# Kernel tuning notes

Hardware: AMD Instinct MI355X
Metric: run time of the kernel (lower is better)

Reference implementation:

```python
import jax, jax.numpy as jnp
import numpy as np

TOP_K = 2
NUM_EXPERTS = 64
TEMPERATURE = 3.0           # buffer initial value (moe_routing_temperature default)
LOAD_BALANCE_ALPHA = 0.01
Z_LOSS_ALPHA = 1e-4


def setup_inputs() -> dict:
    key = jax.random.key(0)
    k1, k2 = jax.random.split(key)
    B, S, H, E = 4, 4096, 4096, NUM_EXPERTS
    x = jax.random.normal(k1, (B, S, H), dtype=jnp.float32)
    gate_w = jax.random.normal(k2, (E, H), dtype=jnp.float32) * (1.0 / np.sqrt(H))
    expert_bias = jnp.zeros((E,), dtype=jnp.float32)
    return {"x": x, "gate_w": gate_w, "expert_bias": expert_bias}


def reference(x, gate_w, expert_bias):
    # Eval-mode path: no noise, no warmup scaling, static top_k, seq_len < 8192
    # -> logits scaled by the temperature buffer.
    B, S, H = x.shape
    E = gate_w.shape[0]
    x_flat = x.reshape(-1, H)                               # [T, H], T = B*S
    logits = jnp.einsum('th,eh->te', x_flat, gate_w) + expert_bias  # [T, E]
    logits = logits / TEMPERATURE
    probs = jax.nn.softmax(logits, axis=-1)                 # [T, E]
    top_scores, top_idx = jax.lax.top_k(probs, TOP_K)       # [T, K]
    top_scores = top_scores / jnp.sum(top_scores, axis=-1, keepdims=True)
    # Load-balance aux loss: fraction of routed tokens per expert * mean prob.
    sel_counts = jax.nn.one_hot(top_idx, E, dtype=logits.dtype).sum(axis=1)  # [T, E]
    frac_routed = sel_counts.mean(axis=0)                   # [E], sums to TOP_K
    mean_prob = probs.mean(axis=0)                          # [E]
    lb_loss = LOAD_BALANCE_ALPHA * E * jnp.sum(frac_routed * mean_prob)
    # Z-loss for routing stability.
    z_loss = Z_LOSS_ALPHA * jnp.mean(jax.nn.logsumexp(logits, axis=-1) ** 2)
    total_loss = lb_loss + z_loss
    return top_scores, top_idx, total_loss
```

## Files before the change

### kernel.cpp

```cpp
#include <hip/hip_runtime.h>
#include <hip/hip_bf16.h>
#include <math.h>

typedef float f32x4 __attribute__((ext_vector_type(4)));
typedef short bf16x8 __attribute__((ext_vector_type(8)));

#define H_DIM 4096
#define E_EXP 64
#define NTOK  16384
#define PLANE (E_EXP * H_DIM)
#define PS    132
#define NBLK  256

__device__ __forceinline__ void split8(f32x4 a, f32x4 b, bf16x8 &h, bf16x8 &m, bf16x8 &l){
#pragma unroll
    for (int j = 0; j < 8; j++){
        float v = (j < 4) ? a[j] : b[j - 4];
        __hip_bfloat16 hb = __float2bfloat16(v);
        float r1 = v - __bfloat162float(hb);
        __hip_bfloat16 mb = __float2bfloat16(r1);
        float r2 = r1 - __bfloat162float(mb);
        __hip_bfloat16 lb = __float2bfloat16(r2);
        h[j] = __builtin_bit_cast(short, hb);
        m[j] = __builtin_bit_cast(short, mb);
        l[j] = __builtin_bit_cast(short, lb);
    }
}

#define MFMA __builtin_amdgcn_mfma_f32_16x16x32_bf16

__device__ __forceinline__ void gload_lds(const short* g, char* l){
    __builtin_amdgcn_global_load_lds(
        (const __attribute__((address_space(1))) void*)g,
        (__attribute__((address_space(3))) void*)l, 16, 0, 0);
}

__global__ __launch_bounds__(256) void moe_wsplit(
    const float* __restrict__ gw, short* __restrict__ wpl)
{
    const int idx = (blockIdx.x * 256 + threadIdx.x) * 8;
    f32x4 a = *(const f32x4*)(gw + idx);
    f32x4 b = *(const f32x4*)(gw + idx + 4);
    bf16x8 h, m, l; split8(a, b, h, m, l);
    *(bf16x8*)(wpl + idx)             = h;
    *(bf16x8*)(wpl + PLANE + idx)     = m;
    *(bf16x8*)(wpl + 2 * PLANE + idx) = l;
}

__global__ __launch_bounds__(256, 3) void moe_gate_main(
    const float* __restrict__ x, const short* __restrict__ wpl,
    const float* __restrict__ bias, float* __restrict__ out,
    float* __restrict__ part)
{
    __shared__ short wlds[12288];
    __shared__ float ls[64 * 68];
    __shared__ float bs[64], rs[64], zW[4];
    __shared__ int   ia[64], ib[64];

    const int tid = threadIdx.x, bid = blockIdx.x;
    const int wv = tid >> 6, l = tid & 63, l16 = l & 15, lk = l >> 4;
    const int tok0 = bid * 64;

    if (tid < 64) bs[tid] = bias[tid];

    const short* wsrc[3]; int wdst[3];
#pragma unroll
    for (int i = 0; i < 3; i++){
        const int sg = wv * 3 + i, p = sg >> 2, kg = sg & 3;
        wsrc[i] = wpl + p * PLANE + l * H_DIM + kg * 8;
        wdst[i] = p * 4096 + kg * 1024;
    }
    const int fb = lk * 1024 + l16 * 16;
    const float* xbase = x + (size_t)(tok0 + wv * 16 + l16) * H_DIM + lk * 8;

    f32x4 acc[4] = {};

#define STAGE(ccn, BUFW) do {                                               \
    __builtin_amdgcn_sched_barrier(0);                                      \
    _Pragma("unroll")                                                       \
    for (int i_ = 0; i_ < 3; i_++)                                          \
        gload_lds(wsrc[i_] + (ccn) * 32,                                    \
                  (char*)wlds + wdst[i_] + (BUFW) * 12288);                 \
    __builtin_amdgcn_sched_barrier(0);                                      \
} while(0)

#define KPHASE(cc, BUFR, XA, XB, XNA, XNB, DO_NEXT) do {                    \
    if (DO_NEXT) {                                                          \
        STAGE((cc) + 1, ((cc) + 1) & 1);                                    \
        XNA = *(const f32x4*)(xbase + ((cc) + 1) * 32);                     \
        XNB = *(const f32x4*)(xbase + ((cc) + 1) * 32 + 4);                 \
    }                                                                       \
    bf16x8 xh, xm, xl; split8(XA, XB, xh, xm, xl);                          \
    bf16x8 wf[4][3];                                                        \
    _Pragma("unroll")                                                       \
    for (int g_ = 0; g_ < 4; g_++)                                          \
        _Pragma("unroll")                                                   \
        for (int p_ = 0; p_ < 3; p_++)                                      \
            wf[g_][p_] = *(const bf16x8*)((char*)wlds + fb +                \
                           (BUFR) * 12288 + p_ * 4096 + g_ * 256);          \
    _Pragma("unroll")                                                       \
    for (int g_ = 0; g_ < 4; g_++){                                         \
        acc[g_] = MFMA(xh, wf[g_][0], acc[g_], 0, 0, 0);                    \
        acc[g_] = MFMA(xm, wf[g_][0], acc[g_], 0, 0, 0);                    \
        acc[g_] = MFMA(xh, wf[g_][1], acc[g_], 0, 0, 0);                    \
        acc[g_] = MFMA(xm, wf[g_][1], acc[g_], 0, 0, 0);                    \
        acc[g_] = MFMA(xh, wf[g_][2], acc[g_], 0, 0, 0);                    \
        acc[g_] = MFMA(xl, wf[g_][0], acc[g_], 0, 0, 0);                    \
    }                                                                       \
    if (DO_NEXT) {                                                          \
        asm volatile("s_waitcnt vmcnt(2)" ::: "memory");                    \
        __builtin_amdgcn_sched_barrier(0);                                  \
        __builtin_amdgcn_s_barrier();                                       \
    }                                                                       \
} while(0)

    STAGE(0, 0);
    f32x4 xeA = *(const f32x4*)(xbase);
    f32x4 xeB = *(const f32x4*)(xbase + 4);
    f32x4 xoA, xoB;
    asm volatile("s_waitcnt vmcnt(2)" ::: "memory");
    __builtin_amdgcn_sched_barrier(0);
    __builtin_amdgcn_s_barrier();

    for (int t = 0; t < 64; t++){
        KPHASE(2 * t,     0, xeA, xeB, xoA, xoB, true);
        KPHASE(2 * t + 1, 1, xoA, xoB, xeA, xeB, (t < 63));
    }

#pragma unroll
    for (int g = 0; g < 4; g++)
#pragma unroll
        for (int r = 0; r < 4; r++)
            ls[(16 * wv + lk * 4 + r) * 68 + g * 16 + l16] = acc[g][r];

    {
        const int t = tid >> 2, s4 = tid & 3, eb0 = s4 * 16;
        const float invTemp = (1.0f / 3.0f);
        float m1 = -1e30f, m2 = -1e30f; int i1 = 0, i2 = 0;
        for (int j = 0; j < 16; ++j){
            const int e = eb0 + j;
            float v = (ls[t * 68 + e] + bs[e]) * invTemp;
            ls[t * 68 + e] = v;
            if (v > m1)      { m2 = m1; i2 = i1; m1 = v; i1 = e; }
            else if (v > m2) { m2 = v;  i2 = e; }
        }
#pragma unroll
        for (int off = 1; off <= 2; off <<= 1){
            float om1 = __shfl_xor(m1, off), om2 = __shfl_xor(m2, off);
            int   oi1 = __shfl_xor(i1, off), oi2 = __shfl_xor(i2, off);
            bool sw = (om1 > m1) || (om1 == m1 && oi1 < i1);
            float n1 = sw ? om1 : m1;  int ni1 = sw ? oi1 : i1;
            float lm = sw ? m1  : om1; int li  = sw ? i1  : oi1;
            float w2 = sw ? om2 : m2;  int wi  = sw ? oi2 : i2;
            bool s2 = (lm > w2) || (lm == w2 && li < wi);
            m1 = n1; i1 = ni1;
            m2 = s2 ? lm : w2; i2 = s2 ? li : wi;
        }
        float ssum = 0.f;
        for (int j = 0; j < 16; ++j){
            const int e = eb0 + j;
            float p = __expf(ls[t * 68 + e] - m1);
            ls[t * 68 + e] = p;
            ssum += p;
        }
        ssum += __shfl_xor(ssum, 1);
        ssum += __shfl_xor(ssum, 2);

        float zsq = 0.f;
        if (s4 == 0){
            rs[t] = 1.0f / ssum; ia[t] = i1; ib[t] = i2;
            float p2    = __expf(m2 - m1);
            float inv12 = 1.0f / (1.0f + p2);
            out[(size_t)(tok0 + t) * 2 + 0] = inv12;
            out[(size_t)(tok0 + t) * 2 + 1] = p2 * inv12;
            out[(size_t)NTOK * 2 + (size_t)(tok0 + t) * 2 + 0] = (float)i1;
            out[(size_t)NTOK * 2 + (size_t)(tok0 + t) * 2 + 1] = (float)i2;
            float lse = m1 + logf(ssum);
            zsq = lse * lse;
        }
#pragma unroll
        for (int o = 32; o; o >>= 1) zsq += __shfl_xor(zsq, o);
        if ((tid & 63) == 0) zW[tid >> 6] = zsq;
    }
    __syncthreads();

    if (tid < 64){
        float psum = 0.f, csum = 0.f;
        for (int t2 = 0; t2 < 64; ++t2){
            psum += ls[t2 * 68 + tid] * rs[t2];
            csum += (ia[t2] == tid ? 1.f : 0.f) + (ib[t2] == tid ? 1.f : 0.f);
        }
        part[bid * PS + tid]      = psum;
        part[bid * PS + 64 + tid] = csum;
        if (tid == 0) part[bid * PS + 128] = zW[0] + zW[1] + zW[2] + zW[3];
    }
}

__global__ __launch_bounds__(1024) void moe_gate_loss(
    const float* __restrict__ part, float* __restrict__ out)
{
    __shared__ float spS[16][64], scS[16][64], zW[16];
    const int tid = threadIdx.x;
    const int e = tid & 63, g = tid >> 6;
    float sp = 0.f, sc = 0.f;
    for (int b = g; b < NBLK; b += 16){
        sp += part[b * PS + e];
        sc += part[b * PS + 64 + e];
    }
    spS[g][e] = sp; scS[g][e] = sc;
    float z = (tid < NBLK) ? part[tid * PS + 128] : 0.f;
#pragma unroll
    for (int o = 32; o; o >>= 1) z += __shfl_xor(z, o);
    if ((tid & 63) == 0) zW[g] = z;
    __syncthreads();

    if (tid < 64){
        float tsp = 0.f, tsc = 0.f;
#pragma unroll
        for (int q = 0; q < 16; ++q){ tsp += spS[q][tid]; tsc += scS[q][tid]; }
        float zp = (tid < 16) ? zW[tid] : 0.f;
        const float invN = 1.0f / (float)NTOK;
        float dot = (tsc * invN) * (tsp * invN);
#pragma unroll
        for (int o = 32; o; o >>= 1){
            dot += __shfl_xor(dot, o);
            zp  += __shfl_xor(zp, o);
        }
        if (tid == 0)
            out[(size_t)NTOK * 4] = 0.01f * 64.0f * dot + 1e-4f * zp * invN;
    }
}

extern "C" void kernel_launch(void* const* d_in, const int* in_sizes, int n_in,
                              void* d_out, int out_size, void* d_ws, size_t ws_size,
                              hipStream_t stream)
{
    const float* x    = (const float*)d_in[0];
    const float* gw   = (const float*)d_in[1];
    const float* bias = (const float*)d_in[2];
    float* out = (float*)d_out;

    short* wpl  = (short*)d_ws;
    float* part = (float*)((char*)d_ws + 3 * PLANE * sizeof(short));

    moe_wsplit<<<128, 256, 0, stream>>>(gw, wpl);
    moe_gate_main<<<NBLK, 256, 0, stream>>>(x, wpl, bias, out, part);
    moe_gate_loss<<<1, 1024, 0, stream>>>(part, out);
}
```

Before: 473.8 us.

## Split gate GEMM over K into four blocks and add combine kernel

The main gating GEMM now launches four times as many blocks, each handling a quarter of the hidden dimension. Each block writes its fp32 partial logits to a workspace buffer. A new combine kernel sums the partials and runs the softmax, top-2, and loss-partial logic that used to sit at the end of the main kernel. This is meant to fill the GPU better, since the old grid gave only about one block per CU. The cost is extra global traffic for the partials and one more kernel launch.

```diff
diff --git a/kernel.cpp b/kernel.cpp
--- a/kernel.cpp
+++ b/kernel.cpp
@@ -10,7 +10,7 @@
 #define NTOK  16384
 #define PLANE (E_EXP * H_DIM)
 #define PS    132
-#define NBLK  256
+#define NCMB  256
 
 __device__ __forceinline__ void split8(f32x4 a, f32x4 b, bf16x8 &h, bf16x8 &m, bf16x8 &l){
 #pragma unroll
@@ -47,31 +47,27 @@
     *(bf16x8*)(wpl + 2 * PLANE + idx) = l;
 }
 
-__global__ __launch_bounds__(256, 3) void moe_gate_main(
+__global__ __launch_bounds__(256, 4) void moe_gate_main(
     const float* __restrict__ x, const short* __restrict__ wpl,
-    const float* __restrict__ bias, float* __restrict__ out,
-    float* __restrict__ part)
+    float* __restrict__ pl)
 {
     __shared__ short wlds[12288];
-    __shared__ float ls[64 * 68];
-    __shared__ float bs[64], rs[64], zW[4];
-    __shared__ int   ia[64], ib[64];
 
     const int tid = threadIdx.x, bid = blockIdx.x;
+    const int tgb = bid >> 2, kq = bid & 3;
     const int wv = tid >> 6, l = tid & 63, l16 = l & 15, lk = l >> 4;
-    const int tok0 = bid * 64;
-
-    if (tid < 64) bs[tid] = bias[tid];
+    const int tok0 = tgb * 64;
+    const int k0 = kq * 1024;
 
     const short* wsrc[3]; int wdst[3];
 #pragma unroll
     for (int i = 0; i < 3; i++){
         const int sg = wv * 3 + i, p = sg >> 2, kg = sg & 3;
-        wsrc[i] = wpl + p * PLANE + l * H_DIM + kg * 8;
+        wsrc[i] = wpl + p * PLANE + l * H_DIM + k0 + kg * 8;
         wdst[i] = p * 4096 + kg * 1024;
     }
     const int fb = lk * 1024 + l16 * 16;
-    const float* xbase = x + (size_t)(tok0 + wv * 16 + l16) * H_DIM + lk * 8;
+    const float* xbase = x + (size_t)(tok0 + wv * 16 + l16) * H_DIM + k0 + lk * 8;
 
     f32x4 acc[4] = {};
 
@@ -122,66 +118,93 @@
     __builtin_amdgcn_sched_barrier(0);
     __builtin_amdgcn_s_barrier();
 
-    for (int t = 0; t < 64; t++){
+    for (int t = 0; t < 16; t++){
         KPHASE(2 * t,     0, xeA, xeB, xoA, xoB, true);
-        KPHASE(2 * t + 1, 1, xoA, xoB, xeA, xeB, (t < 63));
-    }
-
+        KPHASE(2 * t + 1, 1, xoA, xoB, xeA, xeB, (t < 15));
+    }
+
+    float* plb = pl + (size_t)bid * 4096;
 #pragma unroll
     for (int g = 0; g < 4; g++)
 #pragma unroll
         for (int r = 0; r < 4; r++)
-            ls[(16 * wv + lk * 4 + r) * 68 + g * 16 + l16] = acc[g][r];
-
-    {
-        const int t = tid >> 2, s4 = tid & 3, eb0 = s4 * 16;
-        const float invTemp = (1.0f / 3.0f);
-        float m1 = -1e30f, m2 = -1e30f; int i1 = 0, i2 = 0;
-        for (int j = 0; j < 16; ++j){
-            const int e = eb0 + j;
-            float v = (ls[t * 68 + e] + bs[e]) * invTemp;
-            ls[t * 68 + e] = v;
-            if (v > m1)      { m2 = m1; i2 = i1; m1 = v; i1 = e; }
-            else if (v > m2) { m2 = v;  i2 = e; }
-        }
-#pragma unroll
-        for (int off = 1; off <= 2; off <<= 1){
-            float om1 = __shfl_xor(m1, off), om2 = __shfl_xor(m2, off);
-            int   oi1 = __shfl_xor(i1, off), oi2 = __shfl_xor(i2, off);
-            bool sw = (om1 > m1) || (om1 == m1 && oi1 < i1);
-            float n1 = sw ? om1 : m1;  int ni1 = sw ? oi1 : i1;
-            float lm = sw ? m1  : om1; int li  = sw ? i1  : oi1;
-            float w2 = sw ? om2 : m2;  int wi  = sw ? oi2 : i2;
-            bool s2 = (lm > w2) || (lm == w2 && li < wi);
-            m1 = n1; i1 = ni1;
-            m2 = s2 ? lm : w2; i2 = s2 ? li : wi;
-        }
-        float ssum = 0.f;
-        for (int j = 0; j < 16; ++j){
-            const int e = eb0 + j;
-            float p = __expf(ls[t * 68 + e] - m1);
-            ls[t * 68 + e] = p;
-            ssum += p;
-        }
-        ssum += __shfl_xor(ssum, 1);
-        ssum += __shfl_xor(ssum, 2);
-
-        float zsq = 0.f;
-        if (s4 == 0){
-            rs[t] = 1.0f / ssum; ia[t] = i1; ib[t] = i2;
-            float p2    = __expf(m2 - m1);
-            float inv12 = 1.0f / (1.0f + p2);
-            out[(size_t)(tok0 + t) * 2 + 0] = inv12;
-            out[(size_t)(tok0 + t) * 2 + 1] = p2 * inv12;
-            out[(size_t)NTOK * 2 + (size_t)(tok0 + t) * 2 + 0] = (float)i1;
-            out[(size_t)NTOK * 2 + (size_t)(tok0 + t) * 2 + 1] = (float)i2;
-            float lse = m1 + logf(ssum);
-            zsq = lse * lse;
-        }
-#pragma unroll
-        for (int o = 32; o; o >>= 1) zsq += __shfl_xor(zsq, o);
-        if ((tid & 63) == 0) zW[tid >> 6] = zsq;
-    }
+            plb[(16 * wv + lk * 4 + r) * 64 + g * 16 + l16] = acc[g][r];
+}
+
+__global__ __launch_bounds__(256) void moe_combine(
+    const float* __restrict__ pl, const float* __restrict__ bias,
+    float* __restrict__ out, float* __restrict__ part)
+{
+    __shared__ float ls[64 * 68];
+    __shared__ float rs[64], zW[4];
+    __shared__ int   ia[64], ib[64];
+
+    const int tid = threadIdx.x, bid = blockIdx.x;
+    const int tok0 = bid * 64;
+    const int t = tid >> 2, s4 = tid & 3, eb0 = s4 * 16;
+
+    f32x4 bv[4];
+#pragma unroll
+    for (int j = 0; j < 4; j++) bv[j] = *(const f32x4*)(bias + eb0 + 4 * j);
+
+    f32x4 v[4] = {};
+#pragma unroll
+    for (int q = 0; q < 4; q++){
+        const float* p = pl + ((size_t)(bid * 4 + q)) * 4096 + t * 64 + eb0;
+#pragma unroll
+        for (int j = 0; j < 4; j++) v[j] += *(const f32x4*)(p + 4 * j);
+    }
+
+    const float invTemp = (1.0f / 3.0f);
+    float vals[16];
+#pragma unroll
+    for (int j = 0; j < 16; j++)
+        vals[j] = (v[j >> 2][j & 3] + bv[j >> 2][j & 3]) * invTemp;
+
+    float m1 = -1e30f, m2 = -1e30f; int i1 = 0, i2 = 0;
+#pragma unroll
+    for (int j = 0; j < 16; j++){
+        float vv = vals[j]; const int e = eb0 + j;
+        if (vv > m1)      { m2 = m1; i2 = i1; m1 = vv; i1 = e; }
+        else if (vv > m2) { m2 = vv; i2 = e; }
+    }
+#pragma unroll
+    for (int off = 1; off <= 2; off <<= 1){
+        float om1 = __shfl_xor(m1, off), om2 = __shfl_xor(m2, off);
+        int   oi1 = __shfl_xor(i1, off), oi2 = __shfl_xor(i2, off);
+        bool sw = (om1 > m1) || (om1 == m1 && oi1 < i1);
+        float n1 = sw ? om1 : m1;  int ni1 = sw ? oi1 : i1;
+        float lm = sw ? m1  : om1; int li  = sw ? i1  : oi1;
+        float w2 = sw ? om2 : m2;  int wi  = sw ? oi2 : i2;
+        bool s2 = (lm > w2) || (lm == w2 && li < wi);
+        m1 = n1; i1 = ni1;
+        m2 = s2 ? lm : w2; i2 = s2 ? li : wi;
+    }
+    float ssum = 0.f;
+#pragma unroll
+    for (int j = 0; j < 16; j++){
+        float p = __expf(vals[j] - m1);
+        ls[t * 68 + eb0 + j] = p;
+        ssum += p;
+    }
+    ssum += __shfl_xor(ssum, 1);
+    ssum += __shfl_xor(ssum, 2);
+
+    float zsq = 0.f;
+    if (s4 == 0){
+        rs[t] = 1.0f / ssum; ia[t] = i1; ib[t] = i2;
+        float p2    = __expf(m2 - m1);
+        float inv12 = 1.0f / (1.0f + p2);
+        out[(size_t)(tok0 + t) * 2 + 0] = inv12;
+        out[(size_t)(tok0 + t) * 2 + 1] = p2 * inv12;
+        out[(size_t)NTOK * 2 + (size_t)(tok0 + t) * 2 + 0] = (float)i1;
+        out[(size_t)NTOK * 2 + (size_t)(tok0 + t) * 2 + 1] = (float)i2;
+        float lse = m1 + logf(ssum);
+        zsq = lse * lse;
+    }
+#pragma unroll
+    for (int o = 32; o; o >>= 1) zsq += __shfl_xor(zsq, o);
+    if ((tid & 63) == 0) zW[tid >> 6] = zsq;
     __syncthreads();
 
     if (tid < 64){
@@ -203,12 +226,12 @@
     const int tid = threadIdx.x;
     const int e = tid & 63, g = tid >> 6;
     float sp = 0.f, sc = 0.f;
-    for (int b = g; b < NBLK; b += 16){
+    for (int b = g; b < NCMB; b += 16){
         sp += part[b * PS + e];
         sc += part[b * PS + 64 + e];
     }
     spS[g][e] = sp; scS[g][e] = sc;
-    float z = (tid < NBLK) ? part[tid * PS + 128] : 0.f;
+    float z = (tid < NCMB) ? part[tid * PS + 128] : 0.f;
 #pragma unroll
     for (int o = 32; o; o >>= 1) z += __shfl_xor(z, o);
     if ((tid & 63) == 0) zW[g] = z;
@@ -241,9 +264,12 @@
     float* out = (float*)d_out;
 
     short* wpl  = (short*)d_ws;
-    float* part = (float*)((char*)d_ws + 3 * PLANE * sizeof(short));
+    float* pl   = (float*)((char*)d_ws + 3 * PLANE * sizeof(short));
+    float* part = (float*)((char*)d_ws + 3 * PLANE * sizeof(short)
+                           + (size_t)1024 * 4096 * sizeof(float));
 
     moe_wsplit<<<128, 256, 0, stream>>>(gw, wpl);
-    moe_gate_main<<<NBLK, 256, 0, stream>>>(x, wpl, bias, out, part);
+    moe_gate_main<<<1024, 256, 0, stream>>>(x, wpl, pl);
+    moe_combine<<<NCMB, 256, 0, stream>>>(pl, bias, out, part);
     moe_gate_loss<<<1, 1024, 0, stream>>>(part, out);
 }
```

New measurement: 425.8 us. -10.1%, faster.
